# Performance work log

Measured on AMD Instinct MI355X. Metric: run time of the kernel, lower is better.

## Reference

```python
import jax, jax.numpy as jnp
import numpy as np

N_ATOMS = 1048576
N_CRYS = 8192
NFEA = 128
NCLS = 5
LN_EPS = 1e-5


def setup_inputs() -> dict:
    key = jax.random.key(0)
    k1, k2, k3 = jax.random.split(key, 3)
    data_crys_fea = jax.random.normal(k1, (N_ATOMS, NFEA), dtype=jnp.float32)
    # Contiguous non-empty [start, end) ranges partitioning [0, N_ATOMS)
    rng = np.random.default_rng(0)
    cuts = np.sort(rng.choice(np.arange(1, N_ATOMS), size=N_CRYS - 1, replace=False))
    starts = np.concatenate([[0], cuts])
    ends = np.concatenate([cuts, [N_ATOMS]])
    data_crys_idx = jnp.asarray(np.stack([starts, ends], axis=1).astype(np.int32))
    ln_weight = jnp.ones((NFEA,), dtype=jnp.float32)
    ln_bias = jnp.zeros((NFEA,), dtype=jnp.float32)
    out_w = jax.random.normal(k2, (NCLS, NFEA), dtype=jnp.float32) / np.sqrt(NFEA).astype(np.float32)
    out_b = jax.random.normal(k3, (NCLS,), dtype=jnp.float32) * 0.01
    return {
        "data_crys_fea": data_crys_fea,
        "data_crys_idx": data_crys_idx,
        "ln_weight": ln_weight,
        "ln_bias": ln_bias,
        "out_w": out_w,
        "out_b": out_b,
    }


def reference(data_crys_fea, data_crys_idx, ln_weight, ln_bias, out_w, out_b):
    # --- pool: per-crystal mean over contiguous [start, end) atom ranges ---
    starts = data_crys_idx[:, 0]
    ends = data_crys_idx[:, 1]
    n_atoms = data_crys_fea.shape[0]
    # segment id of each atom via searchsorted on sorted starts
    seg = jnp.searchsorted(starts, jnp.arange(n_atoms, dtype=starts.dtype), side="right") - 1
    seg_sum = jax.ops.segment_sum(data_crys_fea, seg, num_segments=N_CRYS)  # [n_crys, F]
    lens = (ends - starts).astype(data_crys_fea.dtype)
    pooled = seg_sum / lens[:, None]
    # --- LayerNorm over features (biased variance, eps=1e-5, like torch) ---
    mu = jnp.mean(pooled, axis=-1, keepdims=True)
    var = jnp.var(pooled, axis=-1, keepdims=True)
    normed = (pooled - mu) / jnp.sqrt(var + LN_EPS) * ln_weight + ln_bias
    # --- Softplus then Linear ---
    act = jax.nn.softplus(normed)  # [n_crys, F]
    my_output = act @ out_w.T + out_b  # [n_crys, n_cls]
    return my_output, act
```

## Files before the change

kernel.cpp:

```cpp
#include <hip/hip_runtime.h>
#include <hip/hip_bf16.h>

#define NFEA 128
#define NCLS 5
#define LN_EPS 1e-5f
#define WCHUNK 64

__global__ __launch_bounds__(256) void prep_kernel(
    const int2* __restrict__ idx,
    int*  __restrict__ seg_of_slab,
    float* __restrict__ seg_sum,
    int n_crys)
{
    const int t    = blockIdx.x * 256 + threadIdx.x;
    const int nthr = gridDim.x * 256;

    float4* z = (float4*)seg_sum;
    const int nz = n_crys * NFEA / 4;
    for (int i = t; i < nz; i += nthr) z[i] = make_float4(0.f, 0.f, 0.f, 0.f);

    if (t < n_crys) {
        const int2 se = idx[t];
        int j = (se.x + WCHUNK - 1) / WCHUNK;
        for (; j * WCHUNK < se.y; ++j) seg_of_slab[j] = t;
    }
}

__global__ __launch_bounds__(256) void seg_partial_kernel(
    const float* __restrict__ fea,
    const int2*  __restrict__ idx,
    const int*   __restrict__ seg_of_slab,
    float* __restrict__ seg_sum)
{
    const int gw   = (blockIdx.x * 256 + threadIdx.x) >> 6;
    const int lane = threadIdx.x & 63;
    const int fc   = lane & 31;
    const int al   = lane >> 5;
    const int a0   = gw * WCHUNK;
    const int a1   = a0 + WCHUNK;

    int s = seg_of_slab[gw];
    const float4* __restrict__ fea4 = (const float4*)fea;

    int rs = a0;
    while (rs < a1) {
        const int re = min(idx[s].y, a1);

        float4 acc0 = make_float4(0.f,0.f,0.f,0.f);
        float4 acc1 = make_float4(0.f,0.f,0.f,0.f);
        float4 acc2 = make_float4(0.f,0.f,0.f,0.f);
        float4 acc3 = make_float4(0.f,0.f,0.f,0.f);

        int a = rs + al;
        if (a + 6 < re) {
            float4 v0 = fea4[(size_t)a       * 32 + fc];
            float4 v1 = fea4[(size_t)(a + 2) * 32 + fc];
            float4 v2 = fea4[(size_t)(a + 4) * 32 + fc];
            float4 v3 = fea4[(size_t)(a + 6) * 32 + fc];
            a += 8;
            for (; a + 6 < re; a += 8) {
                float4 n0 = fea4[(size_t)a       * 32 + fc];
                float4 n1 = fea4[(size_t)(a + 2) * 32 + fc];
                float4 n2 = fea4[(size_t)(a + 4) * 32 + fc];
                float4 n3 = fea4[(size_t)(a + 6) * 32 + fc];
                acc0.x += v0.x; acc0.y += v0.y; acc0.z += v0.z; acc0.w += v0.w;
                acc1.x += v1.x; acc1.y += v1.y; acc1.z += v1.z; acc1.w += v1.w;
                acc2.x += v2.x; acc2.y += v2.y; acc2.z += v2.z; acc2.w += v2.w;
                acc3.x += v3.x; acc3.y += v3.y; acc3.z += v3.z; acc3.w += v3.w;
                v0 = n0; v1 = n1; v2 = n2; v3 = n3;
            }
            acc0.x += v0.x; acc0.y += v0.y; acc0.z += v0.z; acc0.w += v0.w;
            acc1.x += v1.x; acc1.y += v1.y; acc1.z += v1.z; acc1.w += v1.w;
            acc2.x += v2.x; acc2.y += v2.y; acc2.z += v2.z; acc2.w += v2.w;
            acc3.x += v3.x; acc3.y += v3.y; acc3.z += v3.z; acc3.w += v3.w;
        }
        for (; a < re; a += 2) {
            float4 v = fea4[(size_t)a * 32 + fc];
            acc0.x += v.x; acc0.y += v.y; acc0.z += v.z; acc0.w += v.w;
        }

        acc0.x += acc1.x + acc2.x + acc3.x;
        acc0.y += acc1.y + acc2.y + acc3.y;
        acc0.z += acc1.z + acc2.z + acc3.z;
        acc0.w += acc1.w + acc2.w + acc3.w;

        acc0.x += __shfl_xor(acc0.x, 32);
        acc0.y += __shfl_xor(acc0.y, 32);
        acc0.z += __shfl_xor(acc0.z, 32);
        acc0.w += __shfl_xor(acc0.w, 32);

        if (lane < 32) {
            float* dst = &seg_sum[(size_t)s * NFEA + lane * 4];
            atomicAdd(dst + 0, acc0.x);
            atomicAdd(dst + 1, acc0.y);
            atomicAdd(dst + 2, acc0.z);
            atomicAdd(dst + 3, acc0.w);
        }
        rs = re; ++s;
    }
}

__global__ __launch_bounds__(256) void finalize_kernel(
    const float* __restrict__ seg_sum,
    const int2*  __restrict__ idx,
    const float* __restrict__ lnw,
    const float* __restrict__ lnb,
    const float* __restrict__ outw,
    const float* __restrict__ outb,
    float* __restrict__ out_cls,
    float* __restrict__ out_act)
{
    const int c   = (blockIdx.x * 256 + threadIdx.x) >> 6;
    const int tid = threadIdx.x & 63;
    const int2 se = idx[c];
    const float inv_len = 1.f / (float)(se.y - se.x);

    float p0 = seg_sum[(size_t)c * NFEA + tid]      * inv_len;
    float p1 = seg_sum[(size_t)c * NFEA + tid + 64] * inv_len;

    float t = p0 + p1;
    #pragma unroll
    for (int off = 32; off; off >>= 1) t += __shfl_xor(t, off);
    const float mu = t * (1.f / NFEA);

    const float d0 = p0 - mu, d1 = p1 - mu;
    float v = d0 * d0 + d1 * d1;
    #pragma unroll
    for (int off = 32; off; off >>= 1) v += __shfl_xor(v, off);
    const float rstd = rsqrtf(v * (1.f / NFEA) + LN_EPS);

    const float x0 = d0 * rstd * lnw[tid]      + lnb[tid];
    const float x1 = d1 * rstd * lnw[tid + 64] + lnb[tid + 64];
    const float a0 = (x0 > 0.f) ? x0 + log1pf(expf(-x0)) : log1pf(expf(x0));
    const float a1 = (x1 > 0.f) ? x1 + log1pf(expf(-x1)) : log1pf(expf(x1));

    out_act[(size_t)c * NFEA + tid]      = a0;
    out_act[(size_t)c * NFEA + tid + 64] = a1;

    #pragma unroll
    for (int k = 0; k < NCLS; ++k) {
        float p = a0 * outw[k * NFEA + tid] + a1 * outw[k * NFEA + tid + 64];
        #pragma unroll
        for (int off = 32; off; off >>= 1) p += __shfl_xor(p, off);
        if (tid == k) out_cls[(size_t)c * NCLS + k] = p + outb[k];
    }
}

extern "C" void kernel_launch(void* const* d_in, const int* in_sizes, int n_in,
                              void* d_out, int out_size, void* d_ws, size_t ws_size,
                              hipStream_t stream) {
    const float* fea  = (const float*)d_in[0];
    const int2*  idx  = (const int2*)d_in[1];
    const float* lnw  = (const float*)d_in[2];
    const float* lnb  = (const float*)d_in[3];
    const float* outw = (const float*)d_in[4];
    const float* outb = (const float*)d_in[5];

    const int n_crys  = in_sizes[1] / 2;
    const int n_atoms = in_sizes[0] / NFEA;
    const int nslab   = n_atoms / WCHUNK;

    float* seg_sum     = (float*)d_ws;
    int*   seg_of_slab = (int*)((char*)d_ws + (size_t)n_crys * NFEA * sizeof(float));

    float* out_cls = (float*)d_out;
    float* out_act = (float*)d_out + (size_t)n_crys * NCLS;

    prep_kernel<<<128, 256, 0, stream>>>(idx, seg_of_slab, seg_sum, n_crys);
    seg_partial_kernel<<<nslab / 4, 256, 0, stream>>>(fea, idx, seg_of_slab, seg_sum);
    finalize_kernel<<<n_crys / 4, 256, 0, stream>>>(seg_sum, idx, lnw, lnb, outw, outb,
                                                    out_cls, out_act);
}
```

Measured before the change: 129.7 us.

## Fuse finalize into segment-sum for slab-interior crystals, widen slabs, nontemporal loads

```diff
diff --git a/kernel.cpp b/kernel.cpp
--- a/kernel.cpp
+++ b/kernel.cpp
@@ -4,7 +4,51 @@
 #define NFEA 128
 #define NCLS 5
 #define LN_EPS 1e-5f
-#define WCHUNK 64
+#define SLAB 128
+
+typedef float f32x4 __attribute__((ext_vector_type(4)));
+
+__device__ __forceinline__ void finalize_vec(
+    int lane, int fc, int c, f32x4 sum, float inv_len,
+    const float* __restrict__ lnw, const float* __restrict__ lnb,
+    const float* __restrict__ outw, const float* __restrict__ outb,
+    float* __restrict__ out_cls, float* __restrict__ out_act)
+{
+    f32x4 p;
+    p[0] = sum[0] * inv_len; p[1] = sum[1] * inv_len;
+    p[2] = sum[2] * inv_len; p[3] = sum[3] * inv_len;
+
+    float t = p[0] + p[1] + p[2] + p[3];
+    #pragma unroll
+    for (int off = 16; off; off >>= 1) t += __shfl_xor(t, off);
+    const float mu = t * (1.f / NFEA);
+
+    f32x4 d;
+    d[0] = p[0] - mu; d[1] = p[1] - mu; d[2] = p[2] - mu; d[3] = p[3] - mu;
+    float v = d[0]*d[0] + d[1]*d[1] + d[2]*d[2] + d[3]*d[3];
+    #pragma unroll
+    for (int off = 16; off; off >>= 1) v += __shfl_xor(v, off);
+    const float rstd = rsqrtf(v * (1.f / NFEA) + LN_EPS);
+
+    const f32x4 w4 = ((const f32x4*)lnw)[fc];
+    const f32x4 b4 = ((const f32x4*)lnb)[fc];
+    f32x4 act;
+    #pragma unroll
+    for (int j = 0; j < 4; ++j) {
+        const float x = d[j] * rstd * w4[j] + b4[j];
+        act[j] = (x > 0.f) ? x + log1pf(expf(-x)) : log1pf(expf(x));
+    }
+    if (lane < 32) ((f32x4*)out_act)[(size_t)c * 32 + fc] = act;
+
+    #pragma unroll
+    for (int k = 0; k < NCLS; ++k) {
+        const f32x4 wk = ((const f32x4*)outw)[k * 32 + fc];
+        float pk = act[0]*wk[0] + act[1]*wk[1] + act[2]*wk[2] + act[3]*wk[3];
+        #pragma unroll
+        for (int off = 16; off; off >>= 1) pk += __shfl_xor(pk, off);
+        if (lane == k) out_cls[(size_t)c * NCLS + k] = pk + outb[k];
+    }
+}
 
 __global__ __launch_bounds__(256) void prep_kernel(
     const int2* __restrict__ idx,
@@ -15,135 +59,107 @@
     const int t    = blockIdx.x * 256 + threadIdx.x;
     const int nthr = gridDim.x * 256;
 
-    float4* z = (float4*)seg_sum;
+    f32x4* z = (f32x4*)seg_sum;
     const int nz = n_crys * NFEA / 4;
-    for (int i = t; i < nz; i += nthr) z[i] = make_float4(0.f, 0.f, 0.f, 0.f);
+    for (int i = t; i < nz; i += nthr) z[i] = (f32x4){0.f, 0.f, 0.f, 0.f};
 
     if (t < n_crys) {
         const int2 se = idx[t];
-        int j = (se.x + WCHUNK - 1) / WCHUNK;
-        for (; j * WCHUNK < se.y; ++j) seg_of_slab[j] = t;
+        int j = (se.x + SLAB - 1) / SLAB;
+        for (; j * SLAB < se.y; ++j) seg_of_slab[j] = t;
     }
 }
 
-__global__ __launch_bounds__(256) void seg_partial_kernel(
+__global__ __launch_bounds__(256) void main_kernel(
     const float* __restrict__ fea,
     const int2*  __restrict__ idx,
     const int*   __restrict__ seg_of_slab,
-    float* __restrict__ seg_sum)
+    float* __restrict__ seg_sum,
+    const float* __restrict__ lnw, const float* __restrict__ lnb,
+    const float* __restrict__ outw, const float* __restrict__ outb,
+    float* __restrict__ out_cls, float* __restrict__ out_act)
 {
     const int gw   = (blockIdx.x * 256 + threadIdx.x) >> 6;
     const int lane = threadIdx.x & 63;
     const int fc   = lane & 31;
     const int al   = lane >> 5;
-    const int a0   = gw * WCHUNK;
-    const int a1   = a0 + WCHUNK;
+    const int a0   = gw * SLAB;
+    const int a1   = a0 + SLAB;
 
     int s = seg_of_slab[gw];
-    const float4* __restrict__ fea4 = (const float4*)fea;
+    const f32x4* __restrict__ fea4 = (const f32x4*)fea;
 
     int rs = a0;
     while (rs < a1) {
-        const int re = min(idx[s].y, a1);
+        const int2 se = idx[s];
+        const int re = min(se.y, a1);
 
-        float4 acc0 = make_float4(0.f,0.f,0.f,0.f);
-        float4 acc1 = make_float4(0.f,0.f,0.f,0.f);
-        float4 acc2 = make_float4(0.f,0.f,0.f,0.f);
-        float4 acc3 = make_float4(0.f,0.f,0.f,0.f);
+        f32x4 acc0 = {0.f,0.f,0.f,0.f};
+        f32x4 acc1 = {0.f,0.f,0.f,0.f};
+        f32x4 acc2 = {0.f,0.f,0.f,0.f};
+        f32x4 acc3 = {0.f,0.f,0.f,0.f};
 
         int a = rs + al;
         if (a + 6 < re) {
-            float4 v0 = fea4[(size_t)a       * 32 + fc];
-            float4 v1 = fea4[(size_t)(a + 2) * 32 + fc];
-            float4 v2 = fea4[(size_t)(a + 4) * 32 + fc];
-            float4 v3 = fea4[(size_t)(a + 6) * 32 + fc];
+            f32x4 v0 = __builtin_nontemporal_load(fea4 + (size_t)a       * 32 + fc);
+            f32x4 v1 = __builtin_nontemporal_load(fea4 + (size_t)(a + 2) * 32 + fc);
+            f32x4 v2 = __builtin_nontemporal_load(fea4 + (size_t)(a + 4) * 32 + fc);
+            f32x4 v3 = __builtin_nontemporal_load(fea4 + (size_t)(a + 6) * 32 + fc);
             a += 8;
             for (; a + 6 < re; a += 8) {
-                float4 n0 = fea4[(size_t)a       * 32 + fc];
-                float4 n1 = fea4[(size_t)(a + 2) * 32 + fc];
-                float4 n2 = fea4[(size_t)(a + 4) * 32 + fc];
-                float4 n3 = fea4[(size_t)(a + 6) * 32 + fc];
-                acc0.x += v0.x; acc0.y += v0.y; acc0.z += v0.z; acc0.w += v0.w;
-                acc1.x += v1.x; acc1.y += v1.y; acc1.z += v1.z; acc1.w += v1.w;
-                acc2.x += v2.x; acc2.y += v2.y; acc2.z += v2.z; acc2.w += v2.w;
-                acc3.x += v3.x; acc3.y += v3.y; acc3.z += v3.z; acc3.w += v3.w;
+                f32x4 n0 = __builtin_nontemporal_load(fea4 + (size_t)a       * 32 + fc);
+                f32x4 n1 = __builtin_nontemporal_load(fea4 + (size_t)(a + 2) * 32 + fc);
+                f32x4 n2 = __builtin_nontemporal_load(fea4 + (size_t)(a + 4) * 32 + fc);
+                f32x4 n3 = __builtin_nontemporal_load(fea4 + (size_t)(a + 6) * 32 + fc);
+                acc0 += v0; acc1 += v1; acc2 += v2; acc3 += v3;
                 v0 = n0; v1 = n1; v2 = n2; v3 = n3;
             }
-            acc0.x += v0.x; acc0.y += v0.y; acc0.z += v0.z; acc0.w += v0.w;
-            acc1.x += v1.x; acc1.y += v1.y; acc1.z += v1.z; acc1.w += v1.w;
-            acc2.x += v2.x; acc2.y += v2.y; acc2.z += v2.z; acc2.w += v2.w;
-            acc3.x += v3.x; acc3.y += v3.y; acc3.z += v3.z; acc3.w += v3.w;
+            acc0 += v0; acc1 += v1; acc2 += v2; acc3 += v3;
         }
-        for (; a < re; a += 2) {
-            float4 v = fea4[(size_t)a * 32 + fc];
-            acc0.x += v.x; acc0.y += v.y; acc0.z += v.z; acc0.w += v.w;
-        }
+        for (; a < re; a += 2)
+            acc0 += __builtin_nontemporal_load(fea4 + (size_t)a * 32 + fc);
 
-        acc0.x += acc1.x + acc2.x + acc3.x;
-        acc0.y += acc1.y + acc2.y + acc3.y;
-        acc0.z += acc1.z + acc2.z + acc3.z;
-        acc0.w += acc1.w + acc2.w + acc3.w;
+        f32x4 accT = acc0 + acc1;
+        accT += acc2; accT += acc3;
 
-        acc0.x += __shfl_xor(acc0.x, 32);
-        acc0.y += __shfl_xor(acc0.y, 32);
-        acc0.z += __shfl_xor(acc0.z, 32);
-        acc0.w += __shfl_xor(acc0.w, 32);
+        accT[0] += __shfl_xor(accT[0], 32);
+        accT[1] += __shfl_xor(accT[1], 32);
+        accT[2] += __shfl_xor(accT[2], 32);
+        accT[3] += __shfl_xor(accT[3], 32);
 
-        if (lane < 32) {
-            float* dst = &seg_sum[(size_t)s * NFEA + lane * 4];
-            atomicAdd(dst + 0, acc0.x);
-            atomicAdd(dst + 1, acc0.y);
-            atomicAdd(dst + 2, acc0.z);
-            atomicAdd(dst + 3, acc0.w);
+        const bool interior = (se.x >= a0) && (se.y <= a1);
+        if (interior) {
+            finalize_vec(lane, fc, s, accT, 1.f / (float)(se.y - se.x),
+                         lnw, lnb, outw, outb, out_cls, out_act);
+        } else if (lane < 32) {
+            float* dst = &seg_sum[(size_t)s * NFEA + fc * 4];
+            atomicAdd(dst + 0, accT[0]);
+            atomicAdd(dst + 1, accT[1]);
+            atomicAdd(dst + 2, accT[2]);
+            atomicAdd(dst + 3, accT[3]);
         }
         rs = re; ++s;
     }
 }
 
-__global__ __launch_bounds__(256) void finalize_kernel(
+__global__ __launch_bounds__(256) void cleanup_kernel(
     const float* __restrict__ seg_sum,
     const int2*  __restrict__ idx,
-    const float* __restrict__ lnw,
-    const float* __restrict__ lnb,
-    const float* __restrict__ outw,
-    const float* __restrict__ outb,
-    float* __restrict__ out_cls,
-    float* __restrict__ out_act)
+    const float* __restrict__ lnw, const float* __restrict__ lnb,
+    const float* __restrict__ outw, const float* __restrict__ outb,
+    float* __restrict__ out_cls, float* __restrict__ out_act,
+    int n_crys)
 {
-    const int c   = (blockIdx.x * 256 + threadIdx.x) >> 6;
-    const int tid = threadIdx.x & 63;
+    const int c    = (blockIdx.x * 256 + threadIdx.x) >> 6;
+    const int lane = threadIdx.x & 63;
+    if (c >= n_crys) return;
     const int2 se = idx[c];
-    const float inv_len = 1.f / (float)(se.y - se.x);
+    if ((se.x / SLAB) == ((se.y - 1) / SLAB)) return;
 
-    float p0 = seg_sum[(size_t)c * NFEA + tid]      * inv_len;
-    float p1 = seg_sum[(size_t)c * NFEA + tid + 64] * inv_len;
-
-    float t = p0 + p1;
-    #pragma unroll
-    for (int off = 32; off; off >>= 1) t += __shfl_xor(t, off);
-    const float mu = t * (1.f / NFEA);
-
-    const float d0 = p0 - mu, d1 = p1 - mu;
-    float v = d0 * d0 + d1 * d1;
-    #pragma unroll
-    for (int off = 32; off; off >>= 1) v += __shfl_xor(v, off);
-    const float rstd = rsqrtf(v * (1.f / NFEA) + LN_EPS);
-
-    const float x0 = d0 * rstd * lnw[tid]      + lnb[tid];
-    const float x1 = d1 * rstd * lnw[tid + 64] + lnb[tid + 64];
-    const float a0 = (x0 > 0.f) ? x0 + log1pf(expf(-x0)) : log1pf(expf(x0));
-    const float a1 = (x1 > 0.f) ? x1 + log1pf(expf(-x1)) : log1pf(expf(x1));
-
-    out_act[(size_t)c * NFEA + tid]      = a0;
-    out_act[(size_t)c * NFEA + tid + 64] = a1;
-
-    #pragma unroll
-    for (int k = 0; k < NCLS; ++k) {
-        float p = a0 * outw[k * NFEA + tid] + a1 * outw[k * NFEA + tid + 64];
-        #pragma unroll
-        for (int off = 32; off; off >>= 1) p += __shfl_xor(p, off);
-        if (tid == k) out_cls[(size_t)c * NCLS + k] = p + outb[k];
-    }
+    const int fc = lane & 31;
+    const f32x4 sum = ((const f32x4*)seg_sum)[(size_t)c * 32 + fc];
+    finalize_vec(lane, fc, c, sum, 1.f / (float)(se.y - se.x),
+                 lnw, lnb, outw, outb, out_cls, out_act);
 }
 
 extern "C" void kernel_launch(void* const* d_in, const int* in_sizes, int n_in,
@@ -158,7 +174,7 @@
 
     const int n_crys  = in_sizes[1] / 2;
     const int n_atoms = in_sizes[0] / NFEA;
-    const int nslab   = n_atoms / WCHUNK;
+    const int nslab   = n_atoms / SLAB;
 
     float* seg_sum     = (float*)d_ws;
     int*   seg_of_slab = (int*)((char*)d_ws + (size_t)n_crys * NFEA * sizeof(float));
@@ -166,8 +182,10 @@
     float* out_cls = (float*)d_out;
     float* out_act = (float*)d_out + (size_t)n_crys * NCLS;
 
-    prep_kernel<<<128, 256, 0, stream>>>(idx, seg_of_slab, seg_sum, n_crys);
-    seg_partial_kernel<<<nslab / 4, 256, 0, stream>>>(fea, idx, seg_of_slab, seg_sum);
-    finalize_kernel<<<n_crys / 4, 256, 0, stream>>>(seg_sum, idx, lnw, lnb, outw, outb,
-                                                    out_cls, out_act);
+    prep_kernel<<<256, 256, 0, stream>>>(idx, seg_of_slab, seg_sum, n_crys);
+    main_kernel<<<nslab / 4, 256, 0, stream>>>(fea, idx, seg_of_slab, seg_sum,
+                                               lnw, lnb, outw, outb, out_cls, out_act);
+    cleanup_kernel<<<(n_crys + 3) / 4, 256, 0, stream>>>(seg_sum, idx, lnw, lnb,
+                                                         outw, outb, out_cls, out_act,
+                                                         n_crys);
 }
```

New measurement: 140.6 us. 8.4% more time.
